# Kernel optimization log

Hardware: AMD Instinct MI355X
Metric: run time of the kernel (lower is better)

## Reference

```python
import jax, jax.numpy as jnp
import numpy as np

B, T, I, H, NCLU = 512, 64, 64, 128, 5
SCALE = 0.05


def _linear(x, w, b):
    # torch Linear convention: w is [out, in]
    return jnp.einsum('...i,oi->...o', x, w) + b


def _build_adj():
    rng = np.random.RandomState(0)
    feat2clu = rng.randint(0, NCLU, size=I)
    # same-cluster entries = 1 (includes diagonal, which torch also sets to 1)
    adj = (feat2clu[:, None] == feat2clu[None, :]).astype(np.float32)
    return jnp.asarray(adj)


def setup_inputs() -> dict:
    key = jax.random.key(0)
    ks = jax.random.split(key, 20)
    n = lambda k, shape: jax.random.normal(k, shape, jnp.float32) * SCALE
    return {
        'x': jax.random.normal(ks[0], (B, T, I), jnp.float32),
        # stacked per-feature GRU params (input_size=1): ih weight is [I,3H]
        'W_ih': n(ks[1], (I, 3 * H)),
        'W_hh': n(ks[2], (I, 3 * H, H)),
        'b_ih': n(ks[3], (I, 3 * H)),
        'b_hh': n(ks[4], (I, 3 * H)),
        'fp_w': n(ks[5], (H, H)), 'fp_b': n(ks[6], (H,)),
        'g1_w': n(ks[7], (H, H)), 'g1_b': n(ks[8], (H,)),
        'g2_w': n(ks[9], (H, H)), 'g2_b': n(ks[10], (H,)),
        'wq_w': n(ks[11], (H, H)), 'wq_b': n(ks[12], (H,)),
        'wk_w': n(ks[13], (H, H)), 'wk_b': n(ks[14], (H,)),
        'wv_w': n(ks[15], (H, H)), 'wv_b': n(ks[16], (H,)),
        'out0_w': n(ks[17], (H, H)), 'out0_b': n(ks[18], (H,)),
        'adj_mat': _build_adj(),
    }


def _gru_last(x, W_ih, W_hh, b_ih, b_hh):
    # x: [B,T,I]; all I single-input GRUs run as one batched scan over time
    def step(h, xt):  # h: [B,I,H], xt: [B,I]
        gi = xt[:, :, None] * W_ih[None] + b_ih          # [B,I,3H]
        gh = jnp.einsum('bik,igk->big', h, W_hh) + b_hh  # [B,I,3H]
        ir, iz, inn = jnp.split(gi, 3, axis=-1)
        hr, hz, hn = jnp.split(gh, 3, axis=-1)
        r = jax.nn.sigmoid(ir + hr)
        z = jax.nn.sigmoid(iz + hz)
        ncand = jnp.tanh(inn + r * hn)
        h_new = (1.0 - z) * ncand + z * h
        return h_new, None
    h0 = jnp.zeros((x.shape[0], x.shape[2], H), x.dtype)
    hT, _ = jax.lax.scan(step, h0, jnp.moveaxis(x, 1, 0))
    return hT  # [B,I,H] = last visit hidden state per feature


def reference(x, W_ih, W_hh, b_ih, b_hh, fp_w, fp_b, g1_w, g1_b, g2_w, g2_b,
              wq_w, wq_b, wk_w, wk_b, wv_w, wv_b, out0_w, out0_b, adj_mat):
    hs = _gru_last(x, W_ih, W_hh, b_ih, b_hh)          # [B,I,H]
    ht = _linear(hs, fp_w, fp_b)                       # [B,I,H]
    # two-hop adjacency-masked graph conv (dropout = identity in eval)
    g = jax.nn.relu(_linear(jnp.einsum('ij,bjh->bih', adj_mat, ht), g1_w, g1_b))
    ctx = jax.nn.relu(_linear(jnp.einsum('ij,bjh->bih', adj_mat, g), g2_w, g2_b))
    # FinalAttentionQKV, attention_type='mul' over the feature axis
    q = _linear(ctx[:, -1, :], wq_w, wq_b)             # [B,H]
    k = _linear(ctx, wk_w, wk_b)                       # [B,I,H]
    v = _linear(ctx, wv_w, wv_b)                       # [B,I,H]
    e = jnp.einsum('bih,bh->bi', k, q)                 # [B,I]
    a = jax.nn.softmax(e, axis=1)
    wctx = jnp.einsum('bi,bih->bh', a, v)              # [B,H]
    output = jax.nn.relu(_linear(wctx, out0_w, out0_b))
    return output, ht
```

## Files before the change

kernel.cpp:

```cpp
#include <hip/hip_runtime.h>
#include <cstddef>

typedef __bf16 bf16x8 __attribute__((ext_vector_type(8)));
typedef __bf16 bf16x4 __attribute__((ext_vector_type(4)));
typedef float  f32x4  __attribute__((ext_vector_type(4)));

__device__ __forceinline__ float rcp_f(float x)  { return __builtin_amdgcn_rcpf(x); }
__device__ __forceinline__ float exp2_f(float x) { return __builtin_amdgcn_exp2f(x); }

__global__ __launch_bounds__(256, 2) void gru_kernel(
    const float* __restrict__ xg,
    const float* __restrict__ W_ih,
    const float* __restrict__ W_hh,
    const float* __restrict__ b_ih,
    const float* __restrict__ b_hh,
    const float* __restrict__ fp_w,
    const float* __restrict__ fp_b,
    float* __restrict__ ht_out)
{
    __shared__ __align__(16) unsigned char lds[12288];

    const int tid  = threadIdx.x;
    const int wv   = tid >> 6;
    const int lane = tid & 63;
    const int lr   = lane & 15;
    const int lg   = lane >> 4;

    const int bid = blockIdx.x;
    const int f   = ((bid & 7) << 3) | ((bid >> 8) & 7);
    const int m0  = ((bid >> 3) & 31) << 4;

    const int base_ig = f * 384;
    const float s1 = -1.44269504088896f;
    const float s2 = -2.88539008177793f;

    bf16x8 wf[3][2][4];
    #pragma unroll
    for (int g = 0; g < 3; ++g) {
        const float sc = (g == 2) ? s2 : s1;
        #pragma unroll
        for (int nt = 0; nt < 2; ++nt) {
            const float* wrow = W_hh + ((size_t)(base_ig + g*128 + wv*32 + nt*16 + lr)) * 128 + lg*8;
            #pragma unroll
            for (int kt = 0; kt < 4; ++kt) {
                f32x4 w0 = *(const f32x4*)(wrow + kt*32);
                f32x4 w1 = *(const f32x4*)(wrow + kt*32 + 4);
                bf16x8 fr;
                #pragma unroll
                for (int j = 0; j < 4; ++j) { fr[j] = (__bf16)(w0[j]*sc); fr[4+j] = (__bf16)(w1[j]*sc); }
                wf[g][nt][kt] = fr;
            }
        }
    }

    f32x4 WihR[2], WihZ[2], WihN[2], bR[2], bZ[2], bHN[2], bIN[2];
    #pragma unroll
    for (int nt = 0; nt < 2; ++nt) {
        const int n = wv*32 + nt*16 + lg*4;
        f32x4 t0 = *(const f32x4*)(W_ih + base_ig + n);
        f32x4 t1 = *(const f32x4*)(W_ih + base_ig + 128 + n);
        f32x4 t2 = *(const f32x4*)(W_ih + base_ig + 256 + n);
        f32x4 bi0 = *(const f32x4*)(b_ih + base_ig + n);
        f32x4 bi1 = *(const f32x4*)(b_ih + base_ig + 128 + n);
        f32x4 bi2 = *(const f32x4*)(b_ih + base_ig + 256 + n);
        f32x4 bh0 = *(const f32x4*)(b_hh + base_ig + n);
        f32x4 bh1 = *(const f32x4*)(b_hh + base_ig + 128 + n);
        f32x4 bh2 = *(const f32x4*)(b_hh + base_ig + 256 + n);
        #pragma unroll
        for (int j = 0; j < 4; ++j) {
            WihR[nt][j] = t0[j]*s1; WihZ[nt][j] = t1[j]*s1; WihN[nt][j] = t2[j]*s2;
            bR[nt][j]   = (bi0[j]+bh0[j])*s1;
            bZ[nt][j]   = (bi1[j]+bh1[j])*s1;
            bHN[nt][j]  = bh2[j]*s2;
            bIN[nt][j]  = bi2[j]*s2;
        }
    }

    {
        const int m = tid & 15, tq = tid >> 4;
        float* xs = (float*)(lds + 8192);
        const float* xp = xg + (size_t)(m0 + m)*4096 + (size_t)(tq*4)*64 + f;
        #pragma unroll
        for (int tt = 0; tt < 4; ++tt)
            xs[(tq*4 + tt)*16 + m] = xp[tt*64];
    }
    *(f32x4*)(lds + tid*16) = f32x4{0.f,0.f,0.f,0.f};

    const int swm = (lr & 7) << 4;
    int roff[4], woff[2];
    #pragma unroll
    for (int kt = 0; kt < 4; ++kt) roff[kt] = lr*256 + ((kt*64 + lg*16) ^ swm);
    #pragma unroll
    for (int nt = 0; nt < 2; ++nt) woff[nt] = lr*256 + ((wv*64 + nt*32 + lg*8) ^ swm);

    float hreg[2][4] = {{0.f,0.f,0.f,0.f},{0.f,0.f,0.f,0.f}};
    __syncthreads();

    const float* xs = (const float*)(lds + 8192);

#define GRU_STEP(T, CUR, NXT) {                                                   \
    bf16x8 b0 = *(const bf16x8*)(lds + (CUR) + roff[0]);                          \
    bf16x8 b1 = *(const bf16x8*)(lds + (CUR) + roff[1]);                          \
    bf16x8 b2 = *(const bf16x8*)(lds + (CUR) + roff[2]);                          \
    bf16x8 b3 = *(const bf16x8*)(lds + (CUR) + roff[3]);                          \
    f32x4 aR[2], aZ[2], aN[2];                                                    \
    _Pragma("unroll")                                                             \
    for (int nt = 0; nt < 2; ++nt) {                                              \
        aR[nt] = bR[nt]; aZ[nt] = bZ[nt]; aN[nt] = bHN[nt];                       \
        aR[nt] = __builtin_amdgcn_mfma_f32_16x16x32_bf16(wf[0][nt][0], b0, aR[nt], 0,0,0); \
        aR[nt] = __builtin_amdgcn_mfma_f32_16x16x32_bf16(wf[0][nt][1], b1, aR[nt], 0,0,0); \
        aR[nt] = __builtin_amdgcn_mfma_f32_16x16x32_bf16(wf[0][nt][2], b2, aR[nt], 0,0,0); \
        aR[nt] = __builtin_amdgcn_mfma_f32_16x16x32_bf16(wf[0][nt][3], b3, aR[nt], 0,0,0); \
        aZ[nt] = __builtin_amdgcn_mfma_f32_16x16x32_bf16(wf[1][nt][0], b0, aZ[nt], 0,0,0); \
        aZ[nt] = __builtin_amdgcn_mfma_f32_16x16x32_bf16(wf[1][nt][1], b1, aZ[nt], 0,0,0); \
        aZ[nt] = __builtin_amdgcn_mfma_f32_16x16x32_bf16(wf[1][nt][2], b2, aZ[nt], 0,0,0); \
        aZ[nt] = __builtin_amdgcn_mfma_f32_16x16x32_bf16(wf[1][nt][3], b3, aZ[nt], 0,0,0); \
        aN[nt] = __builtin_amdgcn_mfma_f32_16x16x32_bf16(wf[2][nt][0], b0, aN[nt], 0,0,0); \
        aN[nt] = __builtin_amdgcn_mfma_f32_16x16x32_bf16(wf[2][nt][1], b1, aN[nt], 0,0,0); \
        aN[nt] = __builtin_amdgcn_mfma_f32_16x16x32_bf16(wf[2][nt][2], b2, aN[nt], 0,0,0); \
        aN[nt] = __builtin_amdgcn_mfma_f32_16x16x32_bf16(wf[2][nt][3], b3, aN[nt], 0,0,0); \
    }                                                                             \
    const float xv = xs[(T)*16 + lr];                                             \
    _Pragma("unroll")                                                             \
    for (int nt = 0; nt < 2; ++nt) {                                              \
        bf16x4 hw;                                                                \
        _Pragma("unroll")                                                         \
        for (int r = 0; r < 4; ++r) {                                             \
            const float rg = rcp_f(1.f + exp2_f(fmaf(xv, WihR[nt][r], aR[nt][r])));\
            const float zg = rcp_f(1.f + exp2_f(fmaf(xv, WihZ[nt][r], aZ[nt][r])));\
            const float e2 = exp2_f(fmaf(rg, aN[nt][r], fmaf(xv, WihN[nt][r], bIN[nt][r]))); \
            const float nc = (1.f - e2) * rcp_f(1.f + e2);                        \
            float h = hreg[nt][r];                                                \
            h = fmaf(zg, h - nc, nc);                                             \
            hreg[nt][r] = h;                                                      \
            hw[r] = (__bf16)h;                                                    \
        }                                                                         \
        *(bf16x4*)(lds + (NXT) + woff[nt]) = hw;                                  \
    }                                                                             \
    __syncthreads(); }

    #pragma unroll 1
    for (int th = 0; th < 32; ++th) {
        GRU_STEP(2*th,   0,    4096)
        GRU_STEP(2*th+1, 4096, 0)
    }
#undef GRU_STEP

    bf16x8 wo[2][4];
    #pragma unroll
    for (int nt = 0; nt < 2; ++nt) {
        const float* wrow = fp_w + (size_t)(wv*32 + nt*16 + lr) * 128 + lg*8;
        #pragma unroll
        for (int kt = 0; kt < 4; ++kt) {
            f32x4 w0 = *(const f32x4*)(wrow + kt*32);
            f32x4 w1 = *(const f32x4*)(wrow + kt*32 + 4);
            bf16x8 fr;
            #pragma unroll
            for (int j = 0; j < 4; ++j) { fr[j] = (__bf16)w0[j]; fr[4+j] = (__bf16)w1[j]; }
            wo[nt][kt] = fr;
        }
    }
    {
        bf16x8 b0 = *(const bf16x8*)(lds + roff[0]);
        bf16x8 b1 = *(const bf16x8*)(lds + roff[1]);
        bf16x8 b2 = *(const bf16x8*)(lds + roff[2]);
        bf16x8 b3 = *(const bf16x8*)(lds + roff[3]);
        #pragma unroll
        for (int nt = 0; nt < 2; ++nt) {
            f32x4 a2 = *(const f32x4*)(fp_b + wv*32 + nt*16 + lg*4);
            a2 = __builtin_amdgcn_mfma_f32_16x16x32_bf16(wo[nt][0], b0, a2, 0,0,0);
            a2 = __builtin_amdgcn_mfma_f32_16x16x32_bf16(wo[nt][1], b1, a2, 0,0,0);
            a2 = __builtin_amdgcn_mfma_f32_16x16x32_bf16(wo[nt][2], b2, a2, 0,0,0);
            a2 = __builtin_amdgcn_mfma_f32_16x16x32_bf16(wo[nt][3], b3, a2, 0,0,0);
            *(f32x4*)(ht_out + ((size_t)(m0 + lr)*64 + f)*128 + wv*32 + nt*16 + lg*4) = a2;
        }
    }
}

#define NSLOT 8
__global__ __launch_bounds__(128) void tail_kernel(
    const float* __restrict__ ht,
    const float* __restrict__ adj,
    const float* __restrict__ g1_w, const float* __restrict__ g1_b,
    const float* __restrict__ g2_w, const float* __restrict__ g2_b,
    const float* __restrict__ wq_w, const float* __restrict__ wq_b,
    const float* __restrict__ wk_w, const float* __restrict__ wk_b,
    const float* __restrict__ wv_w, const float* __restrict__ wv_b,
    const float* __restrict__ w0_w, const float* __restrict__ w0_b,
    float* __restrict__ outp)
{
    __shared__ float u_s[NSLOT][128];
    __shared__ float g_s[NSLOT][128];
    __shared__ float c_s[NSLOT][128];
    __shared__ float k_s[NSLOT][128];
    __shared__ float q_s[128], w1_s[128], wc_s[128];
    __shared__ int   rep_s[64], slotmap[64], slot[64];
    __shared__ float cntrow[64], cntc[NSLOT], e_s[NSLOT], ca_s[NSLOT];
    __shared__ float sw_s;
    __shared__ int   nrep_s;

    const int tid = threadIdx.x;
    const int b   = blockIdx.x;

    if (tid < 64) {
        int r = 64; float c = 0.f;
        for (int k = 0; k < 64; ++k) {
            float a = adj[tid * 64 + k];
            c += a;
            if (a > 0.5f && k < r) r = k;
        }
        rep_s[tid] = r; cntrow[tid] = c; slotmap[tid] = -1;
    }
    if (tid < NSLOT) cntc[tid] = 0.f;
    __syncthreads();
    if (tid == 0) {
        int n = 0;
        for (int j = 0; j < 64; ++j) {
            int r = rep_s[j];
            int s = slotmap[r];
            if (s < 0) { s = (n < NSLOT) ? n : NSLOT - 1; slotmap[r] = s; cntc[s] = cntrow[r]; ++n; }
            slot[j] = s;
        }
        nrep_s = (n < NSLOT) ? n : NSLOT;
    }
    __syncthreads();
    const int nrep = nrep_s;

    for (int idx = tid; idx < NSLOT * 128; idx += 128) ((float*)u_s)[idx] = 0.f;
    __syncthreads();
    {
        const float* hb = ht + (size_t)b * 8192 + tid;
        for (int j = 0; j < 64; ++j)
            u_s[slot[j]][tid] += hb[j * 128];
    }
    __syncthreads();
    {
        float acc[NSLOT];
        const float bb = g1_b[tid];
        #pragma unroll
        for (int c = 0; c < NSLOT; ++c) acc[c] = bb;
        const f32x4* wr = (const f32x4*)(g1_w + (size_t)tid * 128);
        for (int k4 = 0; k4 < 32; ++k4) {
            const f32x4 w = wr[k4];
            #pragma unroll
            for (int c = 0; c < NSLOT; ++c) {
                const f32x4 u = *(const f32x4*)(&u_s[c][k4 * 4]);
                acc[c] = fmaf(u[0], w[0], acc[c]);
                acc[c] = fmaf(u[1], w[1], acc[c]);
                acc[c] = fmaf(u[2], w[2], acc[c]);
                acc[c] = fmaf(u[3], w[3], acc[c]);
            }
        }
        #pragma unroll
        for (int c = 0; c < NSLOT; ++c) g_s[c][tid] = fmaxf(acc[c], 0.f);
    }
    __syncthreads();
    {
        float acc[NSLOT];
        #pragma unroll
        for (int c = 0; c < NSLOT; ++c) acc[c] = 0.f;
        const f32x4* wr = (const f32x4*)(g2_w + (size_t)tid * 128);
        for (int k4 = 0; k4 < 32; ++k4) {
            const f32x4 w = wr[k4];
            #pragma unroll
            for (int c = 0; c < NSLOT; ++c) {
                const f32x4 g = *(const f32x4*)(&g_s[c][k4 * 4]);
                acc[c] = fmaf(g[0], w[0], acc[c]);
                acc[c] = fmaf(g[1], w[1], acc[c]);
                acc[c] = fmaf(g[2], w[2], acc[c]);
                acc[c] = fmaf(g[3], w[3], acc[c]);
            }
        }
        const float bb = g2_b[tid];
        #pragma unroll
        for (int c = 0; c < NSLOT; ++c) c_s[c][tid] = fmaxf(fmaf(cntc[c], acc[c], bb), 0.f);
    }
    __syncthreads();
    {
        const int s63 = slot[63];
        float acc[NSLOT];
        float qa = wq_b[tid];
        const float bb = wk_b[tid];
        #pragma unroll
        for (int c = 0; c < NSLOT; ++c) acc[c] = bb;
        const f32x4* wr = (const f32x4*)(wk_w + (size_t)tid * 128);
        const f32x4* qr = (const f32x4*)(wq_w + (size_t)tid * 128);
        for (int k4 = 0; k4 < 32; ++k4) {
            const f32x4 w = wr[k4];
            #pragma unroll
            for (int c = 0; c < NSLOT; ++c) {
                const f32x4 v = *(const f32x4*)(&c_s[c][k4 * 4]);
                acc[c] = fmaf(v[0], w[0], acc[c]);
                acc[c] = fmaf(v[1], w[1], acc[c]);
                acc[c] = fmaf(v[2], w[2], acc[c]);
                acc[c] = fmaf(v[3], w[3], acc[c]);
            }
            const f32x4 wq4 = qr[k4];
            const f32x4 xq  = *(const f32x4*)(&c_s[s63][k4 * 4]);
            qa = fmaf(xq[0], wq4[0], qa);
            qa = fmaf(xq[1], wq4[1], qa);
            qa = fmaf(xq[2], wq4[2], qa);
            qa = fmaf(xq[3], wq4[3], qa);
        }
        #pragma unroll
        for (int c = 0; c < NSLOT; ++c) k_s[c][tid] = acc[c];
        q_s[tid] = qa;
    }
    __syncthreads();
    if (tid < NSLOT) {
        float e = 0.f;
        for (int o = 0; o < 128; ++o) e = fmaf(k_s[tid][o], q_s[o], e);
        e_s[tid] = e;
    }
    __syncthreads();
    if (tid == 0) {
        float m = -3.0e38f;
        #pragma unroll
        for (int c = 0; c < NSLOT; ++c) if (c < nrep) m = fmaxf(m, e_s[c]);
        float ex[NSLOT]; float den = 0.f;
        #pragma unroll
        for (int c = 0; c < NSLOT; ++c) { ex[c] = (c < nrep) ? cntc[c] * __expf(e_s[c] - m) : 0.f; den += ex[c]; }
        const float inv = 1.0f / den;
        float sw = 0.f;
        #pragma unroll
        for (int c = 0; c < NSLOT; ++c) { const float a = ex[c] * inv; ca_s[c] = a; sw += a; }
        sw_s = sw;
    }
    __syncthreads();
    {
        float a = 0.f;
        #pragma unroll
        for (int c = 0; c < NSLOT; ++c) a = fmaf(ca_s[c], c_s[c][tid], a);
        w1_s[tid] = a;
    }
    __syncthreads();
    {
        float acc = wv_b[tid] * sw_s;
        const f32x4* wr = (const f32x4*)(wv_w + (size_t)tid * 128);
        for (int k4 = 0; k4 < 32; ++k4) {
            const f32x4 w = wr[k4];
            const f32x4 v = *(const f32x4*)(&w1_s[k4 * 4]);
            acc = fmaf(v[0], w[0], acc);
            acc = fmaf(v[1], w[1], acc);
            acc = fmaf(v[2], w[2], acc);
            acc = fmaf(v[3], w[3], acc);
        }
        wc_s[tid] = acc;
    }
    __syncthreads();
    {
        float acc = w0_b[tid];
        const f32x4* wr = (const f32x4*)(w0_w + (size_t)tid * 128);
        for (int k4 = 0; k4 < 32; ++k4) {
            const f32x4 w = wr[k4];
            const f32x4 v = *(const f32x4*)(&wc_s[k4 * 4]);
            acc = fmaf(v[0], w[0], acc);
            acc = fmaf(v[1], w[1], acc);
            acc = fmaf(v[2], w[2], acc);
            acc = fmaf(v[3], w[3], acc);
        }
        outp[(size_t)b * 128 + tid] = fmaxf(acc, 0.f);
    }
}

extern "C" void kernel_launch(void* const* d_in, const int* in_sizes, int n_in,
                              void* d_out, int out_size, void* d_ws, size_t ws_size,
                              hipStream_t stream) {
    const float* x     = (const float*)d_in[0];
    const float* W_ih  = (const float*)d_in[1];
    const float* W_hh  = (const float*)d_in[2];
    const float* b_ih  = (const float*)d_in[3];
    const float* b_hh  = (const float*)d_in[4];
    const float* fp_w  = (const float*)d_in[5];
    const float* fp_b  = (const float*)d_in[6];
    const float* g1_w  = (const float*)d_in[7];
    const float* g1_b  = (const float*)d_in[8];
    const float* g2_w  = (const float*)d_in[9];
    const float* g2_b  = (const float*)d_in[10];
    const float* wq_w  = (const float*)d_in[11];
    const float* wq_b  = (const float*)d_in[12];
    const float* wk_w  = (const float*)d_in[13];
    const float* wk_b  = (const float*)d_in[14];
    const float* wv_w  = (const float*)d_in[15];
    const float* wv_b  = (const float*)d_in[16];
    const float* o0_w  = (const float*)d_in[17];
    const float* o0_b  = (const float*)d_in[18];
    const float* adj   = (const float*)d_in[19];

    float* outp = (float*)d_out;
    float* ht   = outp + 512 * 128;

    gru_kernel<<<2048, 256, 0, stream>>>(x, W_ih, W_hh, b_ih, b_hh, fp_w, fp_b, ht);
    tail_kernel<<<512, 128, 0, stream>>>(ht, adj, g1_w, g1_b, g2_w, g2_b,
                                         wq_w, wq_b, wk_w, wk_b, wv_w, wv_b,
                                         o0_w, o0_b, outp);
}
```

Baseline: 297.7 us.

## Process four 16-row batch tiles per GRU block to amortize weight loads

Each GRU block now handles 64 batch rows (four 16-row m-tiles) for one feature instead of 16, so the grid shrinks from 2048 to 512 blocks. The per-feature W_hh fragments held in registers are reused across four MFMA tiles, which cuts redundant weight loading and per-step barrier overhead per unit of work. LDS grows to 48KB for the larger hidden-state double buffer and x staging, and hreg quadruples, which raises register pressure and leaves fewer blocks to spread across CUs. The tanh expression is also rewritten as 2*rcp(1+e)-1 to save an instruction.

```diff
diff --git a/kernel.cpp b/kernel.cpp
--- a/kernel.cpp
+++ b/kernel.cpp
@@ -18,7 +18,7 @@
     const float* __restrict__ fp_b,
     float* __restrict__ ht_out)
 {
-    __shared__ __align__(16) unsigned char lds[12288];
+    __shared__ __align__(16) unsigned char lds[49152];
 
     const int tid  = threadIdx.x;
     const int wv   = tid >> 6;
@@ -27,8 +27,8 @@
     const int lg   = lane >> 4;
 
     const int bid = blockIdx.x;
-    const int f   = ((bid & 7) << 3) | ((bid >> 8) & 7);
-    const int m0  = ((bid >> 3) & 31) << 4;
+    const int f   = bid & 63;
+    const int m0  = (bid >> 6) << 6;
 
     const int base_ig = f * 384;
     const float s1 = -1.44269504088896f;
@@ -77,14 +77,18 @@
     }
 
     {
-        const int m = tid & 15, tq = tid >> 4;
-        float* xs = (float*)(lds + 8192);
-        const float* xp = xg + (size_t)(m0 + m)*4096 + (size_t)(tq*4)*64 + f;
-        #pragma unroll
-        for (int tt = 0; tt < 4; ++tt)
-            xs[(tq*4 + tt)*16 + m] = xp[tt*64];
-    }
-    *(f32x4*)(lds + tid*16) = f32x4{0.f,0.f,0.f,0.f};
+        float* xsw = (float*)(lds + 32768);
+        const float* xb = xg + (size_t)m0 * 4096 + f;
+        #pragma unroll
+        for (int tt = 0; tt < 16; ++tt) {
+            const int idx = tt*256 + tid;
+            const int t = idx >> 6, m = idx & 63;
+            xsw[t*64 + m] = xb[(size_t)m*4096 + t*64];
+        }
+    }
+    #pragma unroll
+    for (int j = 0; j < 4; ++j)
+        *(f32x4*)(lds + tid*64 + j*16) = f32x4{0.f,0.f,0.f,0.f};
 
     const int swm = (lr & 7) << 4;
     int roff[4], woff[2];
@@ -93,56 +97,67 @@
     #pragma unroll
     for (int nt = 0; nt < 2; ++nt) woff[nt] = lr*256 + ((wv*64 + nt*32 + lg*8) ^ swm);
 
-    float hreg[2][4] = {{0.f,0.f,0.f,0.f},{0.f,0.f,0.f,0.f}};
-    __syncthreads();
-
-    const float* xs = (const float*)(lds + 8192);
-
-#define GRU_STEP(T, CUR, NXT) {                                                   \
-    bf16x8 b0 = *(const bf16x8*)(lds + (CUR) + roff[0]);                          \
-    bf16x8 b1 = *(const bf16x8*)(lds + (CUR) + roff[1]);                          \
-    bf16x8 b2 = *(const bf16x8*)(lds + (CUR) + roff[2]);                          \
-    bf16x8 b3 = *(const bf16x8*)(lds + (CUR) + roff[3]);                          \
-    f32x4 aR[2], aZ[2], aN[2];                                                    \
+    float hreg[4][2][4];
+    #pragma unroll
+    for (int mt = 0; mt < 4; ++mt)
+        #pragma unroll
+        for (int nt = 0; nt < 2; ++nt)
+            #pragma unroll
+            for (int r = 0; r < 4; ++r) hreg[mt][nt][r] = 0.f;
+
+    __syncthreads();
+
+    const float* xs = (const float*)(lds + 32768);
+
+#define GRU_STEP(T, CUR, NXT)                                                     \
     _Pragma("unroll")                                                             \
-    for (int nt = 0; nt < 2; ++nt) {                                              \
-        aR[nt] = bR[nt]; aZ[nt] = bZ[nt]; aN[nt] = bHN[nt];                       \
-        aR[nt] = __builtin_amdgcn_mfma_f32_16x16x32_bf16(wf[0][nt][0], b0, aR[nt], 0,0,0); \
-        aR[nt] = __builtin_amdgcn_mfma_f32_16x16x32_bf16(wf[0][nt][1], b1, aR[nt], 0,0,0); \
-        aR[nt] = __builtin_amdgcn_mfma_f32_16x16x32_bf16(wf[0][nt][2], b2, aR[nt], 0,0,0); \
-        aR[nt] = __builtin_amdgcn_mfma_f32_16x16x32_bf16(wf[0][nt][3], b3, aR[nt], 0,0,0); \
-        aZ[nt] = __builtin_amdgcn_mfma_f32_16x16x32_bf16(wf[1][nt][0], b0, aZ[nt], 0,0,0); \
-        aZ[nt] = __builtin_amdgcn_mfma_f32_16x16x32_bf16(wf[1][nt][1], b1, aZ[nt], 0,0,0); \
-        aZ[nt] = __builtin_amdgcn_mfma_f32_16x16x32_bf16(wf[1][nt][2], b2, aZ[nt], 0,0,0); \
-        aZ[nt] = __builtin_amdgcn_mfma_f32_16x16x32_bf16(wf[1][nt][3], b3, aZ[nt], 0,0,0); \
-        aN[nt] = __builtin_amdgcn_mfma_f32_16x16x32_bf16(wf[2][nt][0], b0, aN[nt], 0,0,0); \
-        aN[nt] = __builtin_amdgcn_mfma_f32_16x16x32_bf16(wf[2][nt][1], b1, aN[nt], 0,0,0); \
-        aN[nt] = __builtin_amdgcn_mfma_f32_16x16x32_bf16(wf[2][nt][2], b2, aN[nt], 0,0,0); \
-        aN[nt] = __builtin_amdgcn_mfma_f32_16x16x32_bf16(wf[2][nt][3], b3, aN[nt], 0,0,0); \
+    for (int mt = 0; mt < 4; ++mt) {                                              \
+        const int mo = (CUR) + mt*4096;                                           \
+        bf16x8 b0 = *(const bf16x8*)(lds + mo + roff[0]);                         \
+        bf16x8 b1 = *(const bf16x8*)(lds + mo + roff[1]);                         \
+        bf16x8 b2 = *(const bf16x8*)(lds + mo + roff[2]);                         \
+        bf16x8 b3 = *(const bf16x8*)(lds + mo + roff[3]);                         \
+        f32x4 aR[2], aZ[2], aN[2];                                                \
+        _Pragma("unroll")                                                         \
+        for (int nt = 0; nt < 2; ++nt) {                                          \
+            aR[nt] = bR[nt]; aZ[nt] = bZ[nt]; aN[nt] = bHN[nt];                   \
+            aR[nt] = __builtin_amdgcn_mfma_f32_16x16x32_bf16(wf[0][nt][0], b0, aR[nt], 0,0,0); \
+            aR[nt] = __builtin_amdgcn_mfma_f32_16x16x32_bf16(wf[0][nt][1], b1, aR[nt], 0,0,0); \
+            aR[nt] = __builtin_amdgcn_mfma_f32_16x16x32_bf16(wf[0][nt][2], b2, aR[nt], 0,0,0); \
+            aR[nt] = __builtin_amdgcn_mfma_f32_16x16x32_bf16(wf[0][nt][3], b3, aR[nt], 0,0,0); \
+            aZ[nt] = __builtin_amdgcn_mfma_f32_16x16x32_bf16(wf[1][nt][0], b0, aZ[nt], 0,0,0); \
+            aZ[nt] = __builtin_amdgcn_mfma_f32_16x16x32_bf16(wf[1][nt][1], b1, aZ[nt], 0,0,0); \
+            aZ[nt] = __builtin_amdgcn_mfma_f32_16x16x32_bf16(wf[1][nt][2], b2, aZ[nt], 0,0,0); \
+            aZ[nt] = __builtin_amdgcn_mfma_f32_16x16x32_bf16(wf[1][nt][3], b3, aZ[nt], 0,0,0); \
+            aN[nt] = __builtin_amdgcn_mfma_f32_16x16x32_bf16(wf[2][nt][0], b0, aN[nt], 0,0,0); \
+            aN[nt] = __builtin_amdgcn_mfma_f32_16x16x32_bf16(wf[2][nt][1], b1, aN[nt], 0,0,0); \
+            aN[nt] = __builtin_amdgcn_mfma_f32_16x16x32_bf16(wf[2][nt][2], b2, aN[nt], 0,0,0); \
+            aN[nt] = __builtin_amdgcn_mfma_f32_16x16x32_bf16(wf[2][nt][3], b3, aN[nt], 0,0,0); \
+        }                                                                         \
+        const float xv = xs[(T)*64 + mt*16 + lr];                                 \
+        _Pragma("unroll")                                                         \
+        for (int nt = 0; nt < 2; ++nt) {                                          \
+            bf16x4 hw;                                                            \
+            _Pragma("unroll")                                                     \
+            for (int r = 0; r < 4; ++r) {                                         \
+                const float rg = rcp_f(1.f + exp2_f(fmaf(xv, WihR[nt][r], aR[nt][r])));\
+                const float zg = rcp_f(1.f + exp2_f(fmaf(xv, WihZ[nt][r], aZ[nt][r])));\
+                const float e2 = exp2_f(fmaf(rg, aN[nt][r], fmaf(xv, WihN[nt][r], bIN[nt][r]))); \
+                const float nc = fmaf(2.f, rcp_f(1.f + e2), -1.f);                \
+                float h = hreg[mt][nt][r];                                        \
+                h = fmaf(zg, h - nc, nc);                                         \
+                hreg[mt][nt][r] = h;                                              \
+                hw[r] = (__bf16)h;                                                \
+            }                                                                     \
+            *(bf16x4*)(lds + (NXT) + mt*4096 + woff[nt]) = hw;                    \
+        }                                                                         \
     }                                                                             \
-    const float xv = xs[(T)*16 + lr];                                             \
-    _Pragma("unroll")                                                             \
-    for (int nt = 0; nt < 2; ++nt) {                                              \
-        bf16x4 hw;                                                                \
-        _Pragma("unroll")                                                         \
-        for (int r = 0; r < 4; ++r) {                                             \
-            const float rg = rcp_f(1.f + exp2_f(fmaf(xv, WihR[nt][r], aR[nt][r])));\
-            const float zg = rcp_f(1.f + exp2_f(fmaf(xv, WihZ[nt][r], aZ[nt][r])));\
-            const float e2 = exp2_f(fmaf(rg, aN[nt][r], fmaf(xv, WihN[nt][r], bIN[nt][r]))); \
-            const float nc = (1.f - e2) * rcp_f(1.f + e2);                        \
-            float h = hreg[nt][r];                                                \
-            h = fmaf(zg, h - nc, nc);                                             \
-            hreg[nt][r] = h;                                                      \
-            hw[r] = (__bf16)h;                                                    \
-        }                                                                         \
-        *(bf16x4*)(lds + (NXT) + woff[nt]) = hw;                                  \
-    }                                                                             \
-    __syncthreads(); }
+    __syncthreads();
 
     #pragma unroll 1
     for (int th = 0; th < 32; ++th) {
-        GRU_STEP(2*th,   0,    4096)
-        GRU_STEP(2*th+1, 4096, 0)
+        GRU_STEP(2*th,   0,     16384)
+        GRU_STEP(2*th+1, 16384, 0)
     }
 #undef GRU_STEP
 
@@ -160,11 +175,13 @@
             wo[nt][kt] = fr;
         }
     }
-    {
-        bf16x8 b0 = *(const bf16x8*)(lds + roff[0]);
-        bf16x8 b1 = *(const bf16x8*)(lds + roff[1]);
-        bf16x8 b2 = *(const bf16x8*)(lds + roff[2]);
-        bf16x8 b3 = *(const bf16x8*)(lds + roff[3]);
+    #pragma unroll
+    for (int mt = 0; mt < 4; ++mt) {
+        const int mo = mt*4096;
+        bf16x8 b0 = *(const bf16x8*)(lds + mo + roff[0]);
+        bf16x8 b1 = *(const bf16x8*)(lds + mo + roff[1]);
+        bf16x8 b2 = *(const bf16x8*)(lds + mo + roff[2]);
+        bf16x8 b3 = *(const bf16x8*)(lds + mo + roff[3]);
         #pragma unroll
         for (int nt = 0; nt < 2; ++nt) {
             f32x4 a2 = *(const f32x4*)(fp_b + wv*32 + nt*16 + lg*4);
@@ -172,7 +189,7 @@
             a2 = __builtin_amdgcn_mfma_f32_16x16x32_bf16(wo[nt][1], b1, a2, 0,0,0);
             a2 = __builtin_amdgcn_mfma_f32_16x16x32_bf16(wo[nt][2], b2, a2, 0,0,0);
             a2 = __builtin_amdgcn_mfma_f32_16x16x32_bf16(wo[nt][3], b3, a2, 0,0,0);
-            *(f32x4*)(ht_out + ((size_t)(m0 + lr)*64 + f)*128 + wv*32 + nt*16 + lg*4) = a2;
+            *(f32x4*)(ht_out + ((size_t)(m0 + mt*16 + lr)*64 + f)*128 + wv*32 + nt*16 + lg*4) = a2;
         }
     }
 }
@@ -390,7 +407,7 @@
     float* outp = (float*)d_out;
     float* ht   = outp + 512 * 128;
 
-    gru_kernel<<<2048, 256, 0, stream>>>(x, W_ih, W_hh, b_ih, b_hh, fp_w, fp_b, ht);
+    gru_kernel<<<512, 256, 0, stream>>>(x, W_ih, W_hh, b_ih, b_hh, fp_w, fp_b, ht);
     tail_kernel<<<512, 128, 0, stream>>>(ht, adj, g1_w, g1_b, g2_w, g2_b,
                                          wq_w, wq_b, wk_w, wk_b, wv_w, wv_b,
                                          o0_w, o0_b, outp);
```

New measurement: 326.7 us. 1.1x slower.

## Batch GRU gate reciprocals and permute K layout for single 16-byte hidden-state store

Applied to the files above, without the earlier changes.

Replaces per-element reciprocals in the GRU recurrence with a shared-reciprocal trick: products of the (1+exp) denominators are inverted once and individual inverses are recovered by multiplication. This cuts transcendental rcp instructions on the serial critical path. The weight fragments are loaded with a permuted K ordering so each lane's 8 hidden outputs map to contiguous LDS, allowing one bf16x8 store per step instead of two bf16x4 stores. The product-of-denominators trick risks overflow or underflow when exp terms are large, which could produce inf/NaN for saturated gates.

```diff
diff --git a/kernel.cpp b/kernel.cpp
--- a/kernel.cpp
+++ b/kernel.cpp
@@ -40,11 +40,11 @@
         const float sc = (g == 2) ? s2 : s1;
         #pragma unroll
         for (int nt = 0; nt < 2; ++nt) {
-            const float* wrow = W_hh + ((size_t)(base_ig + g*128 + wv*32 + nt*16 + lr)) * 128 + lg*8;
+            const float* wrow = W_hh + ((size_t)(base_ig + g*128 + wv*32 + nt*16 + lr)) * 128;
             #pragma unroll
             for (int kt = 0; kt < 4; ++kt) {
-                f32x4 w0 = *(const f32x4*)(wrow + kt*32);
-                f32x4 w1 = *(const f32x4*)(wrow + kt*32 + 4);
+                f32x4 w0 = *(const f32x4*)(wrow + kt*32 + lg*4);
+                f32x4 w1 = *(const f32x4*)(wrow + kt*32 + 16 + lg*4);
                 bf16x8 fr;
                 #pragma unroll
                 for (int j = 0; j < 4; ++j) { fr[j] = (__bf16)(w0[j]*sc); fr[4+j] = (__bf16)(w1[j]*sc); }
@@ -78,25 +78,25 @@
 
     {
         const int m = tid & 15, tq = tid >> 4;
-        float* xs = (float*)(lds + 8192);
+        float* xsw = (float*)(lds + 8192);
         const float* xp = xg + (size_t)(m0 + m)*4096 + (size_t)(tq*4)*64 + f;
         #pragma unroll
         for (int tt = 0; tt < 4; ++tt)
-            xs[(tq*4 + tt)*16 + m] = xp[tt*64];
+            xsw[(tq*4 + tt)*16 + m] = xp[tt*64];
     }
     *(f32x4*)(lds + tid*16) = f32x4{0.f,0.f,0.f,0.f};
 
     const int swm = (lr & 7) << 4;
-    int roff[4], woff[2];
+    int roff[4];
     #pragma unroll
     for (int kt = 0; kt < 4; ++kt) roff[kt] = lr*256 + ((kt*64 + lg*16) ^ swm);
-    #pragma unroll
-    for (int nt = 0; nt < 2; ++nt) woff[nt] = lr*256 + ((wv*64 + nt*32 + lg*8) ^ swm);
+    const int hwoff = lr*256 + ((wv*64 + lg*16) ^ swm);
 
     float hreg[2][4] = {{0.f,0.f,0.f,0.f},{0.f,0.f,0.f,0.f}};
     __syncthreads();
 
     const float* xs = (const float*)(lds + 8192);
+    const f32x4 one4 = {1.f,1.f,1.f,1.f};
 
 #define GRU_STEP(T, CUR, NXT) {                                                   \
     bf16x8 b0 = *(const bf16x8*)(lds + (CUR) + roff[0]);                          \
@@ -106,37 +106,76 @@
     f32x4 aR[2], aZ[2], aN[2];                                                    \
     _Pragma("unroll")                                                             \
     for (int nt = 0; nt < 2; ++nt) {                                              \
-        aR[nt] = bR[nt]; aZ[nt] = bZ[nt]; aN[nt] = bHN[nt];                       \
-        aR[nt] = __builtin_amdgcn_mfma_f32_16x16x32_bf16(wf[0][nt][0], b0, aR[nt], 0,0,0); \
+        aR[nt] = __builtin_amdgcn_mfma_f32_16x16x32_bf16(wf[0][nt][0], b0, bR[nt], 0,0,0); \
         aR[nt] = __builtin_amdgcn_mfma_f32_16x16x32_bf16(wf[0][nt][1], b1, aR[nt], 0,0,0); \
         aR[nt] = __builtin_amdgcn_mfma_f32_16x16x32_bf16(wf[0][nt][2], b2, aR[nt], 0,0,0); \
         aR[nt] = __builtin_amdgcn_mfma_f32_16x16x32_bf16(wf[0][nt][3], b3, aR[nt], 0,0,0); \
-        aZ[nt] = __builtin_amdgcn_mfma_f32_16x16x32_bf16(wf[1][nt][0], b0, aZ[nt], 0,0,0); \
+        aZ[nt] = __builtin_amdgcn_mfma_f32_16x16x32_bf16(wf[1][nt][0], b0, bZ[nt], 0,0,0); \
         aZ[nt] = __builtin_amdgcn_mfma_f32_16x16x32_bf16(wf[1][nt][1], b1, aZ[nt], 0,0,0); \
         aZ[nt] = __builtin_amdgcn_mfma_f32_16x16x32_bf16(wf[1][nt][2], b2, aZ[nt], 0,0,0); \
         aZ[nt] = __builtin_amdgcn_mfma_f32_16x16x32_bf16(wf[1][nt][3], b3, aZ[nt], 0,0,0); \
-        aN[nt] = __builtin_amdgcn_mfma_f32_16x16x32_bf16(wf[2][nt][0], b0, aN[nt], 0,0,0); \
+        aN[nt] = __builtin_amdgcn_mfma_f32_16x16x32_bf16(wf[2][nt][0], b0, bHN[nt], 0,0,0); \
         aN[nt] = __builtin_amdgcn_mfma_f32_16x16x32_bf16(wf[2][nt][1], b1, aN[nt], 0,0,0); \
         aN[nt] = __builtin_amdgcn_mfma_f32_16x16x32_bf16(wf[2][nt][2], b2, aN[nt], 0,0,0); \
         aN[nt] = __builtin_amdgcn_mfma_f32_16x16x32_bf16(wf[2][nt][3], b3, aN[nt], 0,0,0); \
     }                                                                             \
     const float xv = xs[(T)*16 + lr];                                             \
+    const f32x4 xv4 = {xv, xv, xv, xv};                                           \
+    f32x4 Ap[2], Bp[2];                                                           \
     _Pragma("unroll")                                                             \
     for (int nt = 0; nt < 2; ++nt) {                                              \
-        bf16x4 hw;                                                                \
+        f32x4 gr = xv4*WihR[nt] + aR[nt];                                         \
+        f32x4 gz = xv4*WihZ[nt] + aZ[nt];                                         \
+        f32x4 ea, eb;                                                             \
+        _Pragma("unroll")                                                         \
+        for (int j = 0; j < 4; ++j) { ea[j] = exp2_f(gr[j]); eb[j] = exp2_f(gz[j]); } \
+        Ap[nt] = ea + one4; Bp[nt] = eb + one4;                                   \
+    }                                                                             \
+    f32x4 rg[2], zg[2];                                                           \
+    _Pragma("unroll")                                                             \
+    for (int nt = 0; nt < 2; ++nt) {                                              \
+        const float p01 = Ap[nt][0]*Ap[nt][1];                                    \
+        const float p23 = Bp[nt][0]*Bp[nt][1];                                    \
+        const float rP  = rcp_f(p01*p23);                                         \
+        const float q01 = Ap[nt][2]*Ap[nt][3];                                    \
+        const float q23 = Bp[nt][2]*Bp[nt][3];                                    \
+        const float rQ  = rcp_f(q01*q23);                                         \
+        rg[nt][0] = Ap[nt][1]*p23*rP;                                             \
+        rg[nt][1] = Ap[nt][0]*p23*rP;                                             \
+        zg[nt][0] = p01*Bp[nt][1]*rP;                                             \
+        zg[nt][1] = p01*Bp[nt][0]*rP;                                             \
+        rg[nt][2] = Ap[nt][3]*q23*rQ;                                             \
+        rg[nt][3] = Ap[nt][2]*q23*rQ;                                             \
+        zg[nt][2] = q01*Bp[nt][3]*rQ;                                             \
+        zg[nt][3] = q01*Bp[nt][2]*rQ;                                             \
+    }                                                                             \
+    bf16x8 hw;                                                                    \
+    _Pragma("unroll")                                                             \
+    for (int nt = 0; nt < 2; ++nt) {                                              \
+        f32x4 innv = xv4*WihN[nt] + bIN[nt];                                      \
+        f32x4 arg  = rg[nt]*aN[nt] + innv;                                        \
+        f32x4 e2;                                                                 \
+        _Pragma("unroll")                                                         \
+        for (int j = 0; j < 4; ++j) e2[j] = exp2_f(arg[j]);                       \
+        f32x4 Dp = e2 + one4;                                                     \
+        const float d01 = Dp[0]*Dp[1];                                            \
+        const float d23 = Dp[2]*Dp[3];                                            \
+        const float rD  = rcp_f(d01*d23);                                         \
+        f32x4 invD;                                                               \
+        invD[0] = Dp[1]*d23*rD;                                                   \
+        invD[1] = Dp[0]*d23*rD;                                                   \
+        invD[2] = d01*Dp[3]*rD;                                                   \
+        invD[3] = d01*Dp[2]*rD;                                                   \
         _Pragma("unroll")                                                         \
         for (int r = 0; r < 4; ++r) {                                             \
-            const float rg = rcp_f(1.f + exp2_f(fmaf(xv, WihR[nt][r], aR[nt][r])));\
-            const float zg = rcp_f(1.f + exp2_f(fmaf(xv, WihZ[nt][r], aZ[nt][r])));\
-            const float e2 = exp2_f(fmaf(rg, aN[nt][r], fmaf(xv, WihN[nt][r], bIN[nt][r]))); \
-            const float nc = (1.f - e2) * rcp_f(1.f + e2);                        \
+            const float nc = fmaf(2.f, invD[r], -1.f);                            \
             float h = hreg[nt][r];                                                \
-            h = fmaf(zg, h - nc, nc);                                             \
+            h = fmaf(zg[nt][r], h - nc, nc);                                      \
             hreg[nt][r] = h;                                                      \
-            hw[r] = (__bf16)h;                                                    \
+            hw[nt*4 + r] = (__bf16)h;                                             \
         }                                                                         \
-        *(bf16x4*)(lds + (NXT) + woff[nt]) = hw;                                  \
     }                                                                             \
+    *(bf16x8*)(lds + (NXT) + hwoff) = hw;                                         \
     __syncthreads(); }
 
     #pragma unroll 1
@@ -149,11 +188,11 @@
     bf16x8 wo[2][4];
     #pragma unroll
     for (int nt = 0; nt < 2; ++nt) {
-        const float* wrow = fp_w + (size_t)(wv*32 + nt*16 + lr) * 128 + lg*8;
+        const float* wrow = fp_w + (size_t)(wv*32 + nt*16 + lr) * 128;
         #pragma unroll
         for (int kt = 0; kt < 4; ++kt) {
-            f32x4 w0 = *(const f32x4*)(wrow + kt*32);
-            f32x4 w1 = *(const f32x4*)(wrow + kt*32 + 4);
+            f32x4 w0 = *(const f32x4*)(wrow + kt*32 + lg*4);
+            f32x4 w1 = *(const f32x4*)(wrow + kt*32 + 16 + lg*4);
             bf16x8 fr;
             #pragma unroll
             for (int j = 0; j < 4; ++j) { fr[j] = (__bf16)w0[j]; fr[4+j] = (__bf16)w1[j]; }
```

Result: slower. 321.5 us (+8.0%).
